# Optimization experiments

Hardware: AMD Instinct MI355X
Metric: run time of the kernel (lower is better)

Reference implementation:

```python
import jax, jax.numpy as jnp
import numpy as np

N_NODES = 50000
N_EDGES = 800000
IN_CH = 3
HID = 32
OUT_CH = 16
HEADS = 8
NEG_SLOPE = 0.2  # PyG GATConv default LeakyReLU slope


def setup_inputs() -> dict:
    key = jax.random.key(0)
    ks = jax.random.split(key, 12)
    x = jax.random.normal(ks[0], (N_NODES, IN_CH), dtype=jnp.float32)
    edge_index = jax.random.randint(ks[1], (2, N_EDGES), 0, N_NODES, dtype=jnp.int64)
    # Layer 1: GATConv(3 -> 32, heads=8, concat=True)
    s1 = 1.0 / np.sqrt(IN_CH)
    W1 = jax.random.uniform(ks[2], (IN_CH, HEADS * HID), jnp.float32, -s1, s1)
    att_src1 = jax.random.uniform(ks[3], (HEADS, HID), jnp.float32, -s1, s1)
    att_dst1 = jax.random.uniform(ks[4], (HEADS, HID), jnp.float32, -s1, s1)
    bias1 = jnp.zeros((HEADS * HID,), jnp.float32)
    # Layer 2: GATConv(256 -> 16, heads=1, concat=False)
    s2 = 1.0 / np.sqrt(HEADS * HID)
    W2 = jax.random.uniform(ks[5], (HEADS * HID, 1 * OUT_CH), jnp.float32, -s2, s2)
    att_src2 = jax.random.uniform(ks[6], (1, OUT_CH), jnp.float32, -s2, s2)
    att_dst2 = jax.random.uniform(ks[7], (1, OUT_CH), jnp.float32, -s2, s2)
    bias2 = jnp.zeros((OUT_CH,), jnp.float32)
    return {"x": x, "edge_index": edge_index,
            "W1": W1, "att_src1": att_src1, "att_dst1": att_dst1, "bias1": bias1,
            "W2": W2, "att_src2": att_src2, "att_dst2": att_dst2, "bias2": bias2}


def gat_conv(x, src, dst, W, att_src, att_dst, bias, heads, out_ch, concat):
    """PyG-style GATConv (eval mode: attention dropout is identity).
    src/dst already include self-loops. Returns [N, heads*out_ch] or [N, out_ch]."""
    N = x.shape[0]
    h = (x @ W).reshape(N, heads, out_ch)                      # [N,H,C]
    a_s = jnp.einsum("nhc,hc->nh", h, att_src)                 # [N,H]
    a_d = jnp.einsum("nhc,hc->nh", h, att_dst)                 # [N,H]
    e = jax.nn.leaky_relu(a_s[src] + a_d[dst], NEG_SLOPE)      # [E,H]
    # segment softmax over incoming edges of each dst node
    m = jax.ops.segment_max(e, dst, num_segments=N)            # [N,H]
    e = jnp.exp(e - m[dst])
    denom = jax.ops.segment_sum(e, dst, num_segments=N)        # [N,H]
    alpha = e / (denom[dst] + 1e-16)                           # [E,H]
    msg = h[src] * alpha[:, :, None]                           # [E,H,C]
    out = jax.ops.segment_sum(msg, dst, num_segments=N)        # [N,H,C]
    out = out.reshape(N, heads * out_ch) if concat else out.mean(axis=1)
    return out + bias


def reference(x, edge_index, W1, att_src1, att_dst1, bias1, W2, att_src2, att_dst2, bias2):
    N = x.shape[0]
    loop = jnp.arange(N, dtype=edge_index.dtype)
    src = jnp.concatenate([edge_index[0], loop])  # add self-loops (PyG default)
    dst = jnp.concatenate([edge_index[1], loop])
    h = gat_conv(x, src, dst, W1, att_src1, att_dst1, bias1, HEADS, HID, True)
    h = jax.nn.elu(h)
    out = gat_conv(h, src, dst, W2, att_src2, att_dst2, bias2, 1, OUT_CH, False)
    return out
```

## Files before the change

### kernel.cpp

```cpp
#include <hip/hip_runtime.h>
#include <math.h>

#define N_NODES 50000
#define N_EDGES 800000
#define E_TOT   850000
#define HEADS   8
#define HID     32
#define C1      256
#define OUTC    16
#define NEG     0.2f
#define NBKT    196
#define BCAP    6144
#define EPB     4096
#define NSB     ((E_TOT + EPB - 1) / EPB)

__device__ __forceinline__ float lrelu(float v) { return v > 0.0f ? v : NEG * v; }

__global__ __launch_bounds__(256) void k_setup(
    const float* __restrict__ x, const int* __restrict__ ei,
    const float* __restrict__ W1,
    const float* __restrict__ att_s1, const float* __restrict__ att_d1,
    const float* __restrict__ W2,
    const float* __restrict__ att_s2, const float* __restrict__ att_d2,
    float4* __restrict__ xp,
    unsigned* __restrict__ bucket_cnt, unsigned* __restrict__ ebuf,
    float* __restrict__ As1, float* __restrict__ Ad1,
    float* __restrict__ As2, float* __restrict__ Ad2)
{
    __shared__ unsigned hist[256];
    __shared__ unsigned gpos[256];
    int t = threadIdx.x;
    int blk = blockIdx.x;
    if (blk == 0) {
        if (t < 24) {
            int k = t / 8, h = t % 8;
            float as = 0.0f, ad = 0.0f;
            for (int c = 0; c < HID; c++) {
                float w = W1[k * C1 + h * HID + c];
                as = fmaf(w, att_s1[h * HID + c], as);
                ad = fmaf(w, att_d1[h * HID + c], ad);
            }
            As1[k * 8 + h] = as; Ad1[k * 8 + h] = ad;
        }
        float as2 = 0.0f, ad2 = 0.0f;
        for (int j = 0; j < OUTC; j++) {
            float w = W2[t * OUTC + j];
            as2 = fmaf(w, att_s2[j], as2);
            ad2 = fmaf(w, att_d2[j], ad2);
        }
        As2[t] = as2; Ad2[t] = ad2;
    }
    int nid = blk * 256 + t;
    if (nid < N_NODES)
        xp[nid] = make_float4(x[nid * 3], x[nid * 3 + 1], x[nid * 3 + 2], 1.0f);

    hist[t] = 0;
    __syncthreads();
    unsigned pk[16]; unsigned short rk[16]; unsigned char bk[16];
    int e0 = blk * EPB;
    #pragma unroll
    for (int j = 0; j < 16; j++) {
        int e = e0 + j * 256 + t;
        if (e < E_TOT) {
            int s, d;
            if (e < N_EDGES) { s = ei[e]; d = ei[N_EDGES + e]; }
            else             { s = d = e - N_EDGES; }
            pk[j] = ((unsigned)d << 16) | (unsigned)s;
            int b = d >> 8;
            bk[j] = (unsigned char)b;
            rk[j] = (unsigned short)atomicAdd(&hist[b], 1u);
        } else { pk[j] = 0u; bk[j] = 0; rk[j] = 0; }
    }
    __syncthreads();
    unsigned c = hist[t];
    gpos[t] = c ? atomicAdd(&bucket_cnt[t], c) : 0u;
    __syncthreads();
    #pragma unroll
    for (int j = 0; j < 16; j++) {
        int e = e0 + j * 256 + t;
        if (e < E_TOT) {
            unsigned b = bk[j];
            ebuf[b * BCAP + gpos[b] + rk[j]] = pk[j];
        }
    }
}

__global__ __launch_bounds__(256) void k_csr(
    const unsigned* __restrict__ bucket_cnt, const unsigned* __restrict__ ebuf,
    int* __restrict__ off, unsigned short* __restrict__ csr)
{
    __shared__ unsigned s[256];
    __shared__ unsigned dcnt[256];
    __shared__ unsigned dscan[256];
    int t = threadIdx.x, b = blockIdx.x;
    unsigned cntb = bucket_cnt[b];
    s[t] = (t < NBKT) ? bucket_cnt[t] : 0u;
    dcnt[t] = 0u;
    __syncthreads();
    for (int o = 1; o < 256; o <<= 1) {
        unsigned v = (t >= o) ? s[t - o] : 0u;
        __syncthreads();
        s[t] += v;
        __syncthreads();
    }
    unsigned base = (b == 0) ? 0u : s[b - 1];
    unsigned ev[24]; unsigned short rk[24];
    #pragma unroll
    for (int j = 0; j < 24; j++) {
        int i = j * 256 + t;
        if (i < (int)cntb) {
            unsigned v = ebuf[b * BCAP + i];
            ev[j] = v;
            rk[j] = (unsigned short)atomicAdd(&dcnt[(v >> 16) & 255u], 1u);
        } else { ev[j] = 0u; rk[j] = 0; }
    }
    __syncthreads();
    dscan[t] = dcnt[t];
    __syncthreads();
    for (int o = 1; o < 256; o <<= 1) {
        unsigned v = (t >= o) ? dscan[t - o] : 0u;
        __syncthreads();
        dscan[t] += v;
        __syncthreads();
    }
    int d = b * 256 + t;
    if (d <= N_NODES) off[d] = (int)(base + dscan[t] - dcnt[t]);
    #pragma unroll
    for (int j = 0; j < 24; j++) {
        int i = j * 256 + t;
        if (i < (int)cntb) {
            unsigned d8 = (ev[j] >> 16) & 255u;
            unsigned pos = base + (dscan[d8] - dcnt[d8]) + rk[j];
            csr[pos] = (unsigned short)(ev[j] & 0xFFFFu);
        }
    }
}

__global__ __launch_bounds__(256) void k_agg1(
    const int* __restrict__ off, const unsigned short* __restrict__ csr,
    const float4* __restrict__ xp,
    const float* __restrict__ As1, const float* __restrict__ Ad1,
    float4* __restrict__ xaccw)
{
    int tid = threadIdx.x;
    int h = tid & 7;
    int dst = blockIdx.x * 32 + (tid >> 3);
    if (dst >= N_NODES) return;
    float s0 = As1[h], s1 = As1[8 + h], s2 = As1[16 + h];
    float d0 = Ad1[h], d1 = Ad1[8 + h], d2 = Ad1[16 + h];
    float4 xd = xp[dst];
    float ad = xd.x * d0 + xd.y * d1 + xd.z * d2;
    int beg = off[dst], end = off[dst + 1];
    float a0 = 0.0f, a1 = 0.0f, a2 = 0.0f, a3 = 0.0f;
    int k = beg;
    for (; k + 8 <= end; k += 8) {
        int sm[8]; float4 xv[8];
        #pragma unroll
        for (int j = 0; j < 8; j++) sm[j] = csr[k + j];
        #pragma unroll
        for (int j = 0; j < 8; j++) xv[j] = xp[sm[j]];
        #pragma unroll
        for (int j = 0; j < 8; j++) {
            float as = xv[j].x * s0 + xv[j].y * s1 + xv[j].z * s2;
            float p = __expf(lrelu(as + ad));
            a0 = fmaf(p, xv[j].x, a0);
            a1 = fmaf(p, xv[j].y, a1);
            a2 = fmaf(p, xv[j].z, a2);
            a3 += p;
        }
    }
    if (k < end) {
        int m = end - k;
        int sm[8]; float4 xv[8];
        #pragma unroll
        for (int j = 0; j < 8; j++) { int idx = k + j; sm[j] = csr[idx < end ? idx : k]; }
        #pragma unroll
        for (int j = 0; j < 8; j++) xv[j] = xp[sm[j]];
        #pragma unroll
        for (int j = 0; j < 8; j++) {
            float as = xv[j].x * s0 + xv[j].y * s1 + xv[j].z * s2;
            float p = __expf(lrelu(as + ad));
            p = (j < m) ? p : 0.0f;
            a0 = fmaf(p, xv[j].x, a0);
            a1 = fmaf(p, xv[j].y, a1);
            a2 = fmaf(p, xv[j].z, a2);
            a3 += p;
        }
    }
    xaccw[dst * 8 + h] = make_float4(a0, a1, a2, a3);
}

__global__ __launch_bounds__(256) void k_fin1h2(
    const float4* __restrict__ xaccw, const float* __restrict__ W1,
    const float* __restrict__ b1, const float* __restrict__ W2,
    const float* __restrict__ As2, const float* __restrict__ Ad2,
    float* __restrict__ h2, float* __restrict__ a_s2, float* __restrict__ a_d2)
{
    __shared__ float sW1[3 * C1];
    __shared__ float sAux[3 * C1];
    __shared__ float sW2t[OUTC][260];
    __shared__ float sElu[16][260];
    int t = threadIdx.x;
    for (int i = t; i < 3 * C1; i += 256) sW1[i] = W1[i];
    sAux[t] = b1[t]; sAux[C1 + t] = As2[t]; sAux[2 * C1 + t] = Ad2[t];
    for (int i = t; i < C1 * OUTC; i += 256) {
        int k = i >> 4, j = i & 15;
        sW2t[j][k] = W2[i];
    }
    __syncthreads();
    int n = t >> 4, l = t & 15;
    int node = blockIdx.x * 16 + n;
    float as = 0.0f, ad = 0.0f;
    for (int i = 0; i < 16; i++) {
        int c = l + 16 * i;
        int h = c >> 5;
        float4 xa = xaccw[node * 8 + h];
        float z = (xa.x * sW1[c] + xa.y * sW1[C1 + c] + xa.z * sW1[2 * C1 + c])
                  / (xa.w + 1e-16f) + sAux[c];
        float e = z > 0.0f ? z : expm1f(z);
        sElu[n][c] = e;
        as = fmaf(e, sAux[C1 + c], as);
        ad = fmaf(e, sAux[2 * C1 + c], ad);
    }
    for (int o = 1; o < 16; o <<= 1) {
        as += __shfl_xor(as, o, 64);
        ad += __shfl_xor(ad, o, 64);
    }
    if (l == 0) { a_s2[node] = as; a_d2[node] = ad; }
    __syncthreads();
    const float4* e4 = (const float4*)&sElu[n][0];
    const float4* w4 = (const float4*)&sW2t[l][0];
    float acc = 0.0f;
    #pragma unroll 8
    for (int k = 0; k < 64; k++) {
        float4 a = e4[k], b = w4[k];
        acc = fmaf(a.x, b.x, fmaf(a.y, b.y, fmaf(a.z, b.z, fmaf(a.w, b.w, acc))));
    }
    h2[node * OUTC + l] = acc;
}

__global__ __launch_bounds__(256) void k_agg2(
    const int* __restrict__ off, const unsigned short* __restrict__ csr,
    const float* __restrict__ a_s, const float* __restrict__ a_d,
    const float* __restrict__ h2, const float* __restrict__ bias,
    float* __restrict__ out)
{
    int tid = threadIdx.x;
    int c = tid & 15;
    int dst = blockIdx.x * 16 + (tid >> 4);
    if (dst >= N_NODES) return;
    int beg = off[dst], end = off[dst + 1];
    float ad = a_d[dst];
    float acc = 0.0f, denp = 0.0f;
    int k = beg;
    for (; k + 8 <= end; k += 8) {
        int sm[8]; float p[8];
        #pragma unroll
        for (int j = 0; j < 8; j++) sm[j] = csr[k + j];
        #pragma unroll
        for (int j = 0; j < 8; j++) p[j] = __expf(lrelu(a_s[sm[j]] + ad));
        #pragma unroll
        for (int j = 0; j < 8; j++) {
            denp += p[j];
            acc = fmaf(p[j], h2[sm[j] * OUTC + c], acc);
        }
    }
    if (k < end) {
        int m = end - k;
        int sm[8]; float p[8];
        #pragma unroll
        for (int j = 0; j < 8; j++) { int idx = k + j; sm[j] = csr[idx < end ? idx : k]; }
        #pragma unroll
        for (int j = 0; j < 8; j++) {
            float pj = __expf(lrelu(a_s[sm[j]] + ad));
            p[j] = (j < m) ? pj : 0.0f;
        }
        #pragma unroll
        for (int j = 0; j < 8; j++) {
            denp += p[j];
            acc = fmaf(p[j], h2[sm[j] * OUTC + c], acc);
        }
    }
    out[dst * OUTC + c] = acc / (denp + 1e-16f) + bias[c];
}

extern "C" void kernel_launch(void* const* d_in, const int* in_sizes, int n_in,
                              void* d_out, int out_size, void* d_ws, size_t ws_size,
                              hipStream_t stream)
{
    (void)in_sizes; (void)n_in; (void)out_size; (void)ws_size;
    const float* x    = (const float*)d_in[0];
    const int*   ei   = (const int*)d_in[1];
    const float* W1   = (const float*)d_in[2];
    const float* as1w = (const float*)d_in[3];
    const float* ad1w = (const float*)d_in[4];
    const float* b1   = (const float*)d_in[5];
    const float* W2   = (const float*)d_in[6];
    const float* as2w = (const float*)d_in[7];
    const float* ad2w = (const float*)d_in[8];
    const float* b2   = (const float*)d_in[9];
    float* out = (float*)d_out;

    const long N = N_NODES;
    char* p = (char*)d_ws;
    auto alloc = [&](size_t elems) {
        void* r = p; p += ((elems + 3) & ~(size_t)3) * 4; return r;
    };

    float4*         xp     = (float4*)alloc(N * 4);
    float4*         xaccw  = (float4*)alloc(N * HEADS * 4);
    unsigned*       bcnt   = (unsigned*)alloc(256);
    unsigned*       ebuf   = (unsigned*)alloc((size_t)NBKT * BCAP);
    int*            off    = (int*)alloc(N + 1);
    unsigned short* csr    = (unsigned short*)alloc((E_TOT + 1) / 2);
    float*          As1    = (float*)alloc(32);
    float*          Ad1    = (float*)alloc(32);
    float*          As2    = (float*)alloc(C1);
    float*          Ad2    = (float*)alloc(C1);
    float*          h2v    = (float*)alloc(N * OUTC);
    float*          a_s2   = (float*)alloc(N);
    float*          a_d2   = (float*)alloc(N);

    hipMemsetAsync(bcnt, 0, 256 * sizeof(unsigned), stream);

    k_setup<<<NSB, 256, 0, stream>>>(
        x, ei, W1, as1w, ad1w, W2, as2w, ad2w,
        xp, bcnt, ebuf, As1, Ad1, As2, Ad2);
    k_csr<<<NBKT, 256, 0, stream>>>(bcnt, ebuf, off, csr);
    k_agg1<<<(int)((N + 31) / 32), 256, 0, stream>>>(off, csr, xp, As1, Ad1, xaccw);
    k_fin1h2<<<(int)(N / 16), 256, 0, stream>>>(xaccw, W1, b1, W2, As2, Ad2, h2v, a_s2, a_d2);
    k_agg2<<<(int)((N + 15) / 16), 256, 0, stream>>>(off, csr, a_s2, a_d2, h2v, b2, out);
}
```

Before: 163.2 us.

## Fuse layer-1 aggregation with ELU/projection and drop bucket-count memset

Merges the layer-1 edge aggregation kernel with the finalize/W2 projection kernel, so each 16-thread group handles one node. The two halves of the group split the edge chunks and are combined with shuffles. The h2 projection is computed in registers and reduced with a butterfly shuffle transpose, so the per-node head accumulators no longer round-trip through global memory and one launch is removed. The bucket counter becomes a device global that the fused kernel re-zeroes, replacing the memset. In exchange, every block reloads W2 and W1 into shared memory, per-thread register pressure rises, and correctness across calls now depends on that re-zero.

```diff
diff --git a/kernel.cpp b/kernel.cpp
--- a/kernel.cpp
+++ b/kernel.cpp
@@ -16,14 +16,15 @@
 
 __device__ __forceinline__ float lrelu(float v) { return v > 0.0f ? v : NEG * v; }
 
+__device__ unsigned g_bcnt[256];
+
 __global__ __launch_bounds__(256) void k_setup(
     const float* __restrict__ x, const int* __restrict__ ei,
     const float* __restrict__ W1,
     const float* __restrict__ att_s1, const float* __restrict__ att_d1,
     const float* __restrict__ W2,
     const float* __restrict__ att_s2, const float* __restrict__ att_d2,
-    float4* __restrict__ xp,
-    unsigned* __restrict__ bucket_cnt, unsigned* __restrict__ ebuf,
+    float4* __restrict__ xp, unsigned* __restrict__ ebuf,
     float* __restrict__ As1, float* __restrict__ Ad1,
     float* __restrict__ As2, float* __restrict__ Ad2)
 {
@@ -73,7 +74,7 @@
     }
     __syncthreads();
     unsigned c = hist[t];
-    gpos[t] = c ? atomicAdd(&bucket_cnt[t], c) : 0u;
+    gpos[t] = c ? atomicAdd(&g_bcnt[t], c) : 0u;
     __syncthreads();
     #pragma unroll
     for (int j = 0; j < 16; j++) {
@@ -86,15 +87,15 @@
 }
 
 __global__ __launch_bounds__(256) void k_csr(
-    const unsigned* __restrict__ bucket_cnt, const unsigned* __restrict__ ebuf,
+    const unsigned* __restrict__ ebuf,
     int* __restrict__ off, unsigned short* __restrict__ csr)
 {
     __shared__ unsigned s[256];
     __shared__ unsigned dcnt[256];
     __shared__ unsigned dscan[256];
     int t = threadIdx.x, b = blockIdx.x;
-    unsigned cntb = bucket_cnt[b];
-    s[t] = (t < NBKT) ? bucket_cnt[t] : 0u;
+    unsigned cntb = g_bcnt[b];
+    s[t] = (t < NBKT) ? g_bcnt[t] : 0u;
     dcnt[t] = 0u;
     __syncthreads();
     for (int o = 1; o < 256; o <<= 1) {
@@ -136,24 +137,45 @@
     }
 }
 
-__global__ __launch_bounds__(256) void k_agg1(
+__global__ __launch_bounds__(256) void k_agg1fin(
     const int* __restrict__ off, const unsigned short* __restrict__ csr,
     const float4* __restrict__ xp,
     const float* __restrict__ As1, const float* __restrict__ Ad1,
-    float4* __restrict__ xaccw)
-{
-    int tid = threadIdx.x;
-    int h = tid & 7;
-    int dst = blockIdx.x * 32 + (tid >> 3);
-    if (dst >= N_NODES) return;
+    const float* __restrict__ W1, const float* __restrict__ b1,
+    const float* __restrict__ W2,
+    const float* __restrict__ As2, const float* __restrict__ Ad2,
+    float* __restrict__ h2, float* __restrict__ a_s2, float* __restrict__ a_d2)
+{
+    __shared__ float sP[6 * 256];
+    __shared__ float sW2X[16 * 256];
+    int t = threadIdx.x;
+    if (blockIdx.x == 0) g_bcnt[t] = 0;
+    for (int m = t; m < 6 * 256; m += 256) {
+        int q = m >> 8, i = (m >> 4) & 15, ll = m & 15, c = 16 * ll + i;
+        float v;
+        if (q < 3)       v = W1[q * C1 + c];
+        else if (q == 3) v = b1[c];
+        else if (q == 4) v = As2[c];
+        else             v = Ad2[c];
+        sP[m] = v;
+    }
+    for (int m = t; m < 16 * 256; m += 256) {
+        int i = m >> 8, j = (m >> 4) & 15, ll = m & 15;
+        sW2X[m] = W2[(16 * ll + i) * OUTC + j];
+    }
+    __syncthreads();
+
+    int h = t & 7;
+    int r = (t >> 3) & 1;
+    int l = t & 15;
+    int dst = blockIdx.x * 16 + (t >> 4);
     float s0 = As1[h], s1 = As1[8 + h], s2 = As1[16 + h];
     float d0 = Ad1[h], d1 = Ad1[8 + h], d2 = Ad1[16 + h];
     float4 xd = xp[dst];
     float ad = xd.x * d0 + xd.y * d1 + xd.z * d2;
     int beg = off[dst], end = off[dst + 1];
     float a0 = 0.0f, a1 = 0.0f, a2 = 0.0f, a3 = 0.0f;
-    int k = beg;
-    for (; k + 8 <= end; k += 8) {
+    for (int k = beg + r * 8; k + 8 <= end; k += 16) {
         int sm[8]; float4 xv[8];
         #pragma unroll
         for (int j = 0; j < 8; j++) sm[j] = csr[k + j];
@@ -169,11 +191,13 @@
             a3 += p;
         }
     }
-    if (k < end) {
-        int m = end - k;
+    int nf = (end - beg) & ~7;
+    int ts = beg + nf;
+    if (ts < end && ((nf >> 3) & 1) == r) {
+        int m = end - ts;
         int sm[8]; float4 xv[8];
         #pragma unroll
-        for (int j = 0; j < 8; j++) { int idx = k + j; sm[j] = csr[idx < end ? idx : k]; }
+        for (int j = 0; j < 8; j++) { int idx = ts + j; sm[j] = csr[idx < end ? idx : ts]; }
         #pragma unroll
         for (int j = 0; j < 8; j++) xv[j] = xp[sm[j]];
         #pragma unroll
@@ -187,56 +211,54 @@
             a3 += p;
         }
     }
-    xaccw[dst * 8 + h] = make_float4(a0, a1, a2, a3);
-}
-
-__global__ __launch_bounds__(256) void k_fin1h2(
-    const float4* __restrict__ xaccw, const float* __restrict__ W1,
-    const float* __restrict__ b1, const float* __restrict__ W2,
-    const float* __restrict__ As2, const float* __restrict__ Ad2,
-    float* __restrict__ h2, float* __restrict__ a_s2, float* __restrict__ a_d2)
-{
-    __shared__ float sW1[3 * C1];
-    __shared__ float sAux[3 * C1];
-    __shared__ float sW2t[OUTC][260];
-    __shared__ float sElu[16][260];
-    int t = threadIdx.x;
-    for (int i = t; i < 3 * C1; i += 256) sW1[i] = W1[i];
-    sAux[t] = b1[t]; sAux[C1 + t] = As2[t]; sAux[2 * C1 + t] = Ad2[t];
-    for (int i = t; i < C1 * OUTC; i += 256) {
-        int k = i >> 4, j = i & 15;
-        sW2t[j][k] = W2[i];
-    }
-    __syncthreads();
-    int n = t >> 4, l = t & 15;
-    int node = blockIdx.x * 16 + n;
-    float as = 0.0f, ad = 0.0f;
+    a0 += __shfl_xor(a0, 8, 16);
+    a1 += __shfl_xor(a1, 8, 16);
+    a2 += __shfl_xor(a2, 8, 16);
+    a3 += __shfl_xor(a3, 8, 16);
+
+    float4 xa;
+    xa.x = __shfl(a0, l >> 1, 16);
+    xa.y = __shfl(a1, l >> 1, 16);
+    xa.z = __shfl(a2, l >> 1, 16);
+    xa.w = __shfl(a3, l >> 1, 16);
+    float inv = 1.0f / (xa.w + 1e-16f);
+    float as2a = 0.0f, ad2a = 0.0f;
+    float p[16];
+    #pragma unroll
+    for (int j = 0; j < 16; j++) p[j] = 0.0f;
+    #pragma unroll
     for (int i = 0; i < 16; i++) {
-        int c = l + 16 * i;
-        int h = c >> 5;
-        float4 xa = xaccw[node * 8 + h];
-        float z = (xa.x * sW1[c] + xa.y * sW1[C1 + c] + xa.z * sW1[2 * C1 + c])
-                  / (xa.w + 1e-16f) + sAux[c];
+        float z = fmaf(xa.x, sP[(0 * 16 + i) * 16 + l],
+                  fmaf(xa.y, sP[(1 * 16 + i) * 16 + l],
+                       xa.z * sP[(2 * 16 + i) * 16 + l])) * inv
+                  + sP[(3 * 16 + i) * 16 + l];
         float e = z > 0.0f ? z : expm1f(z);
-        sElu[n][c] = e;
-        as = fmaf(e, sAux[C1 + c], as);
-        ad = fmaf(e, sAux[2 * C1 + c], ad);
-    }
+        as2a = fmaf(e, sP[(4 * 16 + i) * 16 + l], as2a);
+        ad2a = fmaf(e, sP[(5 * 16 + i) * 16 + l], ad2a);
+        #pragma unroll
+        for (int j = 0; j < 16; j++)
+            p[j] = fmaf(e, sW2X[i * 256 + j * 16 + l], p[j]);
+    }
+    #pragma unroll
     for (int o = 1; o < 16; o <<= 1) {
-        as += __shfl_xor(as, o, 64);
-        ad += __shfl_xor(ad, o, 64);
-    }
-    if (l == 0) { a_s2[node] = as; a_d2[node] = ad; }
-    __syncthreads();
-    const float4* e4 = (const float4*)&sElu[n][0];
-    const float4* w4 = (const float4*)&sW2t[l][0];
-    float acc = 0.0f;
-    #pragma unroll 8
-    for (int k = 0; k < 64; k++) {
-        float4 a = e4[k], b = w4[k];
-        acc = fmaf(a.x, b.x, fmaf(a.y, b.y, fmaf(a.z, b.z, fmaf(a.w, b.w, acc))));
-    }
-    h2[node * OUTC + l] = acc;
+        as2a += __shfl_xor(as2a, o, 16);
+        ad2a += __shfl_xor(ad2a, o, 16);
+    }
+    if (l == 0) { a_s2[dst] = as2a; a_d2[dst] = ad2a; }
+    #pragma unroll
+    for (int s = 8; s >= 1; s >>= 1) {
+        bool up = (l & s) != 0;
+        #pragma unroll
+        for (int j = 0; j < 8; j++) {
+            if (j < s) {
+                float send = up ? p[j] : p[j + s];
+                float recv = __shfl_xor(send, s, 16);
+                float keep = up ? p[j + s] : p[j];
+                p[j] = keep + recv;
+            }
+        }
+    }
+    h2[dst * OUTC + l] = p[0];
 }
 
 __global__ __launch_bounds__(256) void k_agg2(
@@ -308,8 +330,6 @@
     };
 
     float4*         xp     = (float4*)alloc(N * 4);
-    float4*         xaccw  = (float4*)alloc(N * HEADS * 4);
-    unsigned*       bcnt   = (unsigned*)alloc(256);
     unsigned*       ebuf   = (unsigned*)alloc((size_t)NBKT * BCAP);
     int*            off    = (int*)alloc(N + 1);
     unsigned short* csr    = (unsigned short*)alloc((E_TOT + 1) / 2);
@@ -321,13 +341,11 @@
     float*          a_s2   = (float*)alloc(N);
     float*          a_d2   = (float*)alloc(N);
 
-    hipMemsetAsync(bcnt, 0, 256 * sizeof(unsigned), stream);
-
     k_setup<<<NSB, 256, 0, stream>>>(
         x, ei, W1, as1w, ad1w, W2, as2w, ad2w,
-        xp, bcnt, ebuf, As1, Ad1, As2, Ad2);
-    k_csr<<<NBKT, 256, 0, stream>>>(bcnt, ebuf, off, csr);
-    k_agg1<<<(int)((N + 31) / 32), 256, 0, stream>>>(off, csr, xp, As1, Ad1, xaccw);
-    k_fin1h2<<<(int)(N / 16), 256, 0, stream>>>(xaccw, W1, b1, W2, As2, Ad2, h2v, a_s2, a_d2);
+        xp, ebuf, As1, Ad1, As2, Ad2);
+    k_csr<<<NBKT, 256, 0, stream>>>(ebuf, off, csr);
+    k_agg1fin<<<(int)(N / 16), 256, 0, stream>>>(
+        off, csr, xp, As1, Ad1, W1, b1, W2, As2, Ad2, h2v, a_s2, a_d2);
     k_agg2<<<(int)((N + 15) / 16), 256, 0, stream>>>(off, csr, a_s2, a_d2, h2v, b2, out);
 }
```

New measurement: 270.6 us. +65.9%, slower.
